# Performance work log

Hardware: AMD Instinct MI355X
Metric: run time of the kernel (lower is better)

## Reference

```python
import jax, jax.numpy as jnp
import numpy as np

R = 1.1
SCALE = 100.0
BUMP_STEPS = 32
NUM_THETAS = 32
NUM_FEATURES = 128
N_NODES = 200000
NUM_GRAPHS = 128


def setup_inputs() -> dict:
    key = jax.random.key(0)
    k1, k2, k3 = jax.random.split(key, 3)
    x = jax.random.normal(k1, (N_NODES, NUM_FEATURES), dtype=jnp.float32)
    batch = jnp.sort(jax.random.randint(k2, (N_NODES,), 0, NUM_GRAPHS, dtype=jnp.int64))
    v = jax.random.uniform(k3, (NUM_THETAS, NUM_FEATURES), dtype=jnp.float32) - 0.5
    return {"x": x, "batch": batch, "num_graphs": NUM_GRAPHS, "v": v}


def reference(x, batch, num_graphs, v):
    # nh: node heights along each direction theta -> [N, T]
    nh = x @ v.T
    # linspace over filtration values -> [S]
    lin = jnp.linspace(-R, R, BUMP_STEPS, dtype=nh.dtype)
    # bump: sigmoid difference; second point is the constant pad value R
    # ecc: [N, S, T]  (node-major so segment_sum reduces the leading axis)
    ecc = (jax.nn.sigmoid(SCALE * (lin[None, :, None] - nh[:, None, :]))
           - jax.nn.sigmoid(SCALE * (lin - R))[None, :, None])
    # scatter-add per graph label -> [ng, S, T] == index_add over dim1 then movedim(0,1)
    ect = jax.ops.segment_sum(ecc, batch, num_segments=num_graphs)
    return ect
```

## Files before the change

kernel.cpp:

```cpp
#include <hip/hip_runtime.h>
#include <math.h>

#define N_NODES 200000
#define NF 128
#define NT 32
#define NS 32
#define NG 128
#define ATILE 64
#define ABLOCKS 3125
#define VSTRIDE 136
#define HPAD 33

typedef short bf16x8 __attribute__((ext_vector_type(8)));
typedef float floatx4 __attribute__((ext_vector_type(4)));

__device__ __forceinline__ float rcp_fast(float x) { return __builtin_amdgcn_rcpf(x); }

__device__ __forceinline__ void split_bf16(float f, unsigned short& h, unsigned short& l) {
    unsigned u  = __float_as_uint(f);
    unsigned r  = u + 0x7FFFu + ((u >> 16) & 1u);
    unsigned hb = r & 0xFFFF0000u;
    h = (unsigned short)(hb >> 16);
    float rem = f - __uint_as_float(hb);
    unsigned u2 = __float_as_uint(rem);
    unsigned r2 = u2 + 0x7FFFu + ((u2 >> 16) & 1u);
    l = (unsigned short)(r2 >> 16);
}

__device__ __forceinline__ void split8(float4 a, float4 b, bf16x8& h8, bf16x8& l8) {
    unsigned short h[8], l[8];
    split_bf16(a.x, h[0], l[0]); split_bf16(a.y, h[1], l[1]);
    split_bf16(a.z, h[2], l[2]); split_bf16(a.w, h[3], l[3]);
    split_bf16(b.x, h[4], l[4]); split_bf16(b.y, h[5], l[5]);
    split_bf16(b.z, h[6], l[6]); split_bf16(b.w, h[7], l[7]);
    h8 = (bf16x8){(short)h[0],(short)h[1],(short)h[2],(short)h[3],
                  (short)h[4],(short)h[5],(short)h[6],(short)h[7]};
    l8 = (bf16x8){(short)l[0],(short)l[1],(short)l[2],(short)l[3],
                  (short)l[4],(short)l[5],(short)l[6],(short)l[7]};
}

__global__ __launch_bounds__(256, 4)
void ect_fused(const float* __restrict__ x,
               const int* __restrict__ batch,
               const float* __restrict__ v,
               float* __restrict__ out)
{
    __shared__ unsigned short vh[NT * VSTRIDE];
    __shared__ unsigned short vl[NT * VSTRIDE];
    __shared__ int      batch_lds[ATILE];
    __shared__ unsigned hist[NT * HPAD];
    __shared__ float    corr[NT * HPAD];
    __shared__ float    cnt_lds;

    const int tid  = threadIdx.x;
    const int blk  = blockIdx.x;
    const int w    = tid >> 6;
    const int lane = tid & 63;
    const int mrow = lane & 15;
    const int quad = lane >> 4;

    #pragma unroll
    for (int j = 0; j < 4; ++j) {
        int idx4 = j * 256 + tid;
        int row  = idx4 >> 5;
        int f4   = idx4 & 31;
        float4 val = *(const float4*)&v[(size_t)row * NF + f4 * 4];
        unsigned short h0,h1,h2,h3,l0,l1,l2,l3;
        split_bf16(val.x, h0, l0); split_bf16(val.y, h1, l1);
        split_bf16(val.z, h2, l2); split_bf16(val.w, h3, l3);
        uint2 hh, ll;
        hh.x = (unsigned)h0 | ((unsigned)h1 << 16); hh.y = (unsigned)h2 | ((unsigned)h3 << 16);
        ll.x = (unsigned)l0 | ((unsigned)l1 << 16); ll.y = (unsigned)l2 | ((unsigned)l3 << 16);
        *(uint2*)&vh[row * VSTRIDE + f4 * 4] = hh;
        *(uint2*)&vl[row * VSTRIDE + f4 * 4] = ll;
    }
    if (tid < ATILE) batch_lds[tid] = batch[blk * ATILE + tid];

    const size_t arow = (size_t)blk * ATILE + w * 16 + mrow;
    const float* __restrict__ xrow = x + arow * NF + quad * 8;

    floatx4 acc0 = {0.f, 0.f, 0.f, 0.f};
    floatx4 acc1 = {0.f, 0.f, 0.f, 0.f};

    bf16x8 ah[4], al[4];
    #pragma unroll
    for (int slice = 0; slice < 4; ++slice) {
        float4 a0 = *(const float4*)&xrow[slice * 32];
        float4 a1 = *(const float4*)&xrow[slice * 32 + 4];
        split8(a0, a1, ah[slice], al[slice]);
    }
    __syncthreads();

    const int b0base = mrow * VSTRIDE + quad * 8;
    const int b1base = (16 + mrow) * VSTRIDE + quad * 8;
    #pragma unroll
    for (int slice = 0; slice < 4; ++slice) {
        bf16x8 bh0 = *(bf16x8*)&vh[b0base + slice * 32];
        bf16x8 bl0 = *(bf16x8*)&vl[b0base + slice * 32];
        bf16x8 bh1 = *(bf16x8*)&vh[b1base + slice * 32];
        bf16x8 bl1 = *(bf16x8*)&vl[b1base + slice * 32];
        acc0 = __builtin_amdgcn_mfma_f32_16x16x32_bf16(ah[slice], bh0, acc0, 0, 0, 0);
        acc0 = __builtin_amdgcn_mfma_f32_16x16x32_bf16(ah[slice], bl0, acc0, 0, 0, 0);
        acc0 = __builtin_amdgcn_mfma_f32_16x16x32_bf16(al[slice], bh0, acc0, 0, 0, 0);
        acc1 = __builtin_amdgcn_mfma_f32_16x16x32_bf16(ah[slice], bh1, acc1, 0, 0, 0);
        acc1 = __builtin_amdgcn_mfma_f32_16x16x32_bf16(ah[slice], bl1, acc1, 0, 0, 0);
        acc1 = __builtin_amdgcn_mfma_f32_16x16x32_bf16(al[slice], bh1, acc1, 0, 0, 0);
    }

    const float inv_dlin = 14.090909090909092f;
    const float Lw       = 10.23848093f;
    const float dlin     = 2.2f / 31.0f;
    const float L        = 144.26950408889634f;

    const int g_first = batch_lds[0];
    const int g_last  = batch_lds[ATILE - 1];

    const int ft = tid & 31;
    const int sb = tid >> 5;

    for (int gp = g_first; gp <= g_last; ++gp) {
        for (int i = tid; i < NT * HPAD; i += 256) { hist[i] = 0u; corr[i] = 0.0f; }
        __syncthreads();

        #pragma unroll
        for (int reg = 0; reg < 4; ++reg) {
            int n = w * 16 + quad * 4 + reg;
            if (batch_lds[n] == gp) {
                #pragma unroll
                for (int half = 0; half < 2; ++half) {
                    int   t = half ? (16 + mrow) : mrow;
                    float h = half ? acc1[reg] : acc0[reg];
                    float z = fmaf(h, inv_dlin, 15.5f);
                    int s_up = (int)ceilf(z);
                    s_up = min(max(s_up, 0), 32);
                    atomicAdd(&hist[t * HPAD + s_up], 1u);
                    int s0 = (int)ceilf(z - 1.45f);
                    #pragma unroll
                    for (int i2 = 0; i2 < 3; ++i2) {
                        int s = s0 + i2;
                        float e   = __builtin_amdgcn_exp2f(Lw * (z - (float)s));
                        float sig = rcp_fast(1.0f + e);
                        float stp = (s >= s_up) ? 1.0f : 0.0f;
                        if (s >= 0 && s <= 31) atomicAdd(&corr[t * HPAD + s], sig - stp);
                    }
                }
            }
        }
        __syncthreads();

        if (tid < ATILE) {
            unsigned long long m = __ballot(batch_lds[tid] == gp);
            if (tid == 0) cnt_lds = (float)__popcll(m);
        }
        {
            const int grp = tid >> 5;
            const int s   = tid & 31;
            for (int row = grp; row < NT; row += 8) {
                float val = (float)hist[row * HPAD + s];
                #pragma unroll
                for (int d = 1; d < 32; d <<= 1) {
                    float nbr = __shfl_up(val, d, 32);
                    if (s >= d) val += nbr;
                }
                corr[row * HPAD + s] += val;
            }
        }
        __syncthreads();

        #pragma unroll
        for (int k = 0; k < 4; ++k) {
            int s = sb + 8 * k;
            float lin_s = -1.1f + (float)s * dlin;
            float cs  = rcp_fast(1.0f + __builtin_amdgcn_exp2f(L * (1.1f - lin_s)));
            float val = corr[ft * HPAD + s] - cnt_lds * cs;
            atomicAdd(&out[(size_t)gp * (NS * NT) + s * NT + ft], val);
        }
        if (gp < g_last) __syncthreads();
    }
}

extern "C" void kernel_launch(void* const* d_in, const int* in_sizes, int n_in,
                              void* d_out, int out_size, void* d_ws, size_t ws_size,
                              hipStream_t stream) {
    const float* x     = (const float*)d_in[0];
    const int*   batch = (const int*)d_in[1];
    const float* v     = (const float*)d_in[3];
    float*       out   = (float*)d_out;

    hipMemsetAsync(d_out, 0, (size_t)out_size * sizeof(float), stream);
    ect_fused<<<dim3(ABLOCKS), dim3(256), 0, stream>>>(x, batch, v, out);
}
```

Before: 168.8 us.

## Precompute bf16 split of v in a prep kernel and drop LDS staging

Moves the per-block hi/lo bf16 split of v into a small separate kernel that writes to workspace, so the main kernel reads B fragments straight from global/L2 instead of staging them through LDS behind a barrier. Batch labels are also read from global into registers instead of LDS, and the occupancy hint is raised from 4 to 6 blocks per CU since LDS use drops. This cuts redundant conversion work across 3125 blocks and an early barrier, at the cost of an extra launch and uncoalesced-ish global fragment loads that rely on cache hits.

```diff
diff --git a/kernel.cpp b/kernel.cpp
--- a/kernel.cpp
+++ b/kernel.cpp
@@ -8,7 +8,6 @@
 #define NG 128
 #define ATILE 64
 #define ABLOCKS 3125
-#define VSTRIDE 136
 #define HPAD 33
 
 typedef short bf16x8 __attribute__((ext_vector_type(8)));
@@ -39,15 +38,28 @@
                   (short)l[4],(short)l[5],(short)l[6],(short)l[7]};
 }
 
-__global__ __launch_bounds__(256, 4)
+__global__ __launch_bounds__(256)
+void prep_v(const float* __restrict__ v,
+            unsigned short* __restrict__ vh,
+            unsigned short* __restrict__ vl)
+{
+    int j = blockIdx.x * 256 + threadIdx.x;
+    if (j >= NT * NF / 4) return;
+    float4 val = ((const float4*)v)[j];
+    unsigned short h0,h1,h2,h3,l0,l1,l2,l3;
+    split_bf16(val.x, h0, l0); split_bf16(val.y, h1, l1);
+    split_bf16(val.z, h2, l2); split_bf16(val.w, h3, l3);
+    ((ushort4*)vh)[j] = make_ushort4(h0, h1, h2, h3);
+    ((ushort4*)vl)[j] = make_ushort4(l0, l1, l2, l3);
+}
+
+__global__ __launch_bounds__(256, 6)
 void ect_fused(const float* __restrict__ x,
                const int* __restrict__ batch,
-               const float* __restrict__ v,
+               const unsigned short* __restrict__ vh,
+               const unsigned short* __restrict__ vl,
                float* __restrict__ out)
 {
-    __shared__ unsigned short vh[NT * VSTRIDE];
-    __shared__ unsigned short vl[NT * VSTRIDE];
-    __shared__ int      batch_lds[ATILE];
     __shared__ unsigned hist[NT * HPAD];
     __shared__ float    corr[NT * HPAD];
     __shared__ float    cnt_lds;
@@ -59,28 +71,8 @@
     const int mrow = lane & 15;
     const int quad = lane >> 4;
 
-    #pragma unroll
-    for (int j = 0; j < 4; ++j) {
-        int idx4 = j * 256 + tid;
-        int row  = idx4 >> 5;
-        int f4   = idx4 & 31;
-        float4 val = *(const float4*)&v[(size_t)row * NF + f4 * 4];
-        unsigned short h0,h1,h2,h3,l0,l1,l2,l3;
-        split_bf16(val.x, h0, l0); split_bf16(val.y, h1, l1);
-        split_bf16(val.z, h2, l2); split_bf16(val.w, h3, l3);
-        uint2 hh, ll;
-        hh.x = (unsigned)h0 | ((unsigned)h1 << 16); hh.y = (unsigned)h2 | ((unsigned)h3 << 16);
-        ll.x = (unsigned)l0 | ((unsigned)l1 << 16); ll.y = (unsigned)l2 | ((unsigned)l3 << 16);
-        *(uint2*)&vh[row * VSTRIDE + f4 * 4] = hh;
-        *(uint2*)&vl[row * VSTRIDE + f4 * 4] = ll;
-    }
-    if (tid < ATILE) batch_lds[tid] = batch[blk * ATILE + tid];
-
     const size_t arow = (size_t)blk * ATILE + w * 16 + mrow;
     const float* __restrict__ xrow = x + arow * NF + quad * 8;
-
-    floatx4 acc0 = {0.f, 0.f, 0.f, 0.f};
-    floatx4 acc1 = {0.f, 0.f, 0.f, 0.f};
 
     bf16x8 ah[4], al[4];
     #pragma unroll
@@ -89,16 +81,17 @@
         float4 a1 = *(const float4*)&xrow[slice * 32 + 4];
         split8(a0, a1, ah[slice], al[slice]);
     }
-    __syncthreads();
 
-    const int b0base = mrow * VSTRIDE + quad * 8;
-    const int b1base = (16 + mrow) * VSTRIDE + quad * 8;
+    floatx4 acc0 = {0.f, 0.f, 0.f, 0.f};
+    floatx4 acc1 = {0.f, 0.f, 0.f, 0.f};
+    const int b0off = mrow * NF + quad * 8;
+    const int b1off = (16 + mrow) * NF + quad * 8;
     #pragma unroll
     for (int slice = 0; slice < 4; ++slice) {
-        bf16x8 bh0 = *(bf16x8*)&vh[b0base + slice * 32];
-        bf16x8 bl0 = *(bf16x8*)&vl[b0base + slice * 32];
-        bf16x8 bh1 = *(bf16x8*)&vh[b1base + slice * 32];
-        bf16x8 bl1 = *(bf16x8*)&vl[b1base + slice * 32];
+        bf16x8 bh0 = *(const bf16x8*)&vh[b0off + slice * 32];
+        bf16x8 bl0 = *(const bf16x8*)&vl[b0off + slice * 32];
+        bf16x8 bh1 = *(const bf16x8*)&vh[b1off + slice * 32];
+        bf16x8 bl1 = *(const bf16x8*)&vl[b1off + slice * 32];
         acc0 = __builtin_amdgcn_mfma_f32_16x16x32_bf16(ah[slice], bh0, acc0, 0, 0, 0);
         acc0 = __builtin_amdgcn_mfma_f32_16x16x32_bf16(ah[slice], bl0, acc0, 0, 0, 0);
         acc0 = __builtin_amdgcn_mfma_f32_16x16x32_bf16(al[slice], bh0, acc0, 0, 0, 0);
@@ -107,13 +100,18 @@
         acc1 = __builtin_amdgcn_mfma_f32_16x16x32_bf16(al[slice], bh1, acc1, 0, 0, 0);
     }
 
+    const int base = blk * ATILE;
+    const int g_first = batch[base];
+    const int g_last  = batch[base + ATILE - 1];
+    int nlabel[4];
+    #pragma unroll
+    for (int reg = 0; reg < 4; ++reg)
+        nlabel[reg] = batch[base + w * 16 + quad * 4 + reg];
+
     const float inv_dlin = 14.090909090909092f;
     const float Lw       = 10.23848093f;
     const float dlin     = 2.2f / 31.0f;
     const float L        = 144.26950408889634f;
-
-    const int g_first = batch_lds[0];
-    const int g_last  = batch_lds[ATILE - 1];
 
     const int ft = tid & 31;
     const int sb = tid >> 5;
@@ -124,8 +122,7 @@
 
         #pragma unroll
         for (int reg = 0; reg < 4; ++reg) {
-            int n = w * 16 + quad * 4 + reg;
-            if (batch_lds[n] == gp) {
+            if (nlabel[reg] == gp) {
                 #pragma unroll
                 for (int half = 0; half < 2; ++half) {
                     int   t = half ? (16 + mrow) : mrow;
@@ -149,7 +146,7 @@
         __syncthreads();
 
         if (tid < ATILE) {
-            unsigned long long m = __ballot(batch_lds[tid] == gp);
+            unsigned long long m = __ballot(batch[base + tid] == gp);
             if (tid == 0) cnt_lds = (float)__popcll(m);
         }
         {
@@ -187,6 +184,10 @@
     const float* v     = (const float*)d_in[3];
     float*       out   = (float*)d_out;
 
+    unsigned short* vh = (unsigned short*)d_ws;
+    unsigned short* vl = vh + NT * NF;
+
     hipMemsetAsync(d_out, 0, (size_t)out_size * sizeof(float), stream);
-    ect_fused<<<dim3(ABLOCKS), dim3(256), 0, stream>>>(x, batch, v, out);
+    prep_v<<<dim3(4), dim3(256), 0, stream>>>(v, vh, vl);
+    ect_fused<<<dim3(ABLOCKS), dim3(256), 0, stream>>>(x, batch, vh, vl, out);
 }
```

Result: no change. 170.8 us (+1.2%).
